# Optimization experiments

Hardware: AMD Instinct MI355X
Metric: run time of the kernel (lower is better)

Reference implementation:

```python
import jax, jax.numpy as jnp
import numpy as np

B, C, N, M_MODES, EMB = 8, 64, 2048, 32, 256
MFREQ = 2 * M_MODES * (2 * M_MODES - 1)  # 4032
SCALE = 1.0 / (C * C)


def setup_inputs() -> dict:
    key = jax.random.key(0)
    ks = jax.random.split(key, 16)
    d = {
        "x": jax.random.normal(ks[0], (B, C, N), jnp.float32),
        "emb": jax.random.normal(ks[1], (B, EMB), jnp.float32),
        "Vf_re": jax.random.normal(ks[2], (MFREQ, N), jnp.float32),
        "Vf_im": jax.random.normal(ks[3], (MFREQ, N), jnp.float32),
        "Vi_re": jax.random.normal(ks[4], (N, MFREQ), jnp.float32),
        "Vi_im": jax.random.normal(ks[5], (N, MFREQ), jnp.float32),
        "w1_re": SCALE * jax.random.uniform(ks[6], (C, C, M_MODES, M_MODES), jnp.float32),
        "w1_im": SCALE * jax.random.uniform(ks[7], (C, C, M_MODES, M_MODES), jnp.float32),
        "w2_re": SCALE * jax.random.uniform(ks[8], (C, C, M_MODES, M_MODES), jnp.float32),
        "w2_im": SCALE * jax.random.uniform(ks[9], (C, C, M_MODES, M_MODES), jnp.float32),
        "m1_re": SCALE * jax.random.uniform(ks[10], (1, M_MODES, M_MODES, EMB), jnp.float32),
        "m1_im": SCALE * jax.random.uniform(ks[11], (1, M_MODES, M_MODES, EMB), jnp.float32),
        "m2_re": SCALE * jax.random.uniform(ks[12], (1, M_MODES, M_MODES, EMB), jnp.float32),
        "m2_im": SCALE * jax.random.uniform(ks[13], (1, M_MODES, M_MODES, EMB), jnp.float32),
    }
    return d


def _spectral_conv(x, emb, Vf, Vi, w1, w2, mod1, mod2):
    m = M_MODES
    # nuft.forward: [B,N,C] complex -> [B,MFREQ,C]
    xc = jnp.transpose(x, (0, 2, 1)).astype(jnp.complex64)
    x_nfft = jnp.einsum('mn,bnc->bmc', Vf, xc)
    # [B,C,2m,2m-1]
    x_ft = jnp.transpose(x_nfft, (0, 2, 1)).reshape(x.shape[0], C, 2 * m, 2 * m - 1)
    embc = emb.astype(jnp.complex64)[:, None, None, :]  # [B,1,1,EMB]
    phi1 = jnp.sum(mod1 * embc, axis=-1)  # [B,m,m]
    phi2 = jnp.sum(mod2 * embc, axis=-1)
    out1 = jnp.einsum('bixy,ioxy->boxy', x_ft[:, :, :m, :m], w1)
    out2 = jnp.einsum('bixy,ioxy->boxy', x_ft[:, :, -m:, :m], w2)
    mod1b = phi1[:, None, :, :] * out1
    mod2b = phi2[:, None, :, :] * out2
    out_ft = jnp.concatenate([mod1b, mod2b], axis=2)  # [B,C,2m,m]
    xf = out_ft.reshape(x.shape[0], C, 2 * m * m)
    # Hermitian-symmetry reconstruction: flip over mode AND channel dims, conj
    xf2 = jnp.conj(jnp.flip(xf[..., 2 * m:], axis=(-2, -1)))
    xf = jnp.concatenate([xf, xf2], axis=-1)  # [B,C,MFREQ]
    xf = jnp.transpose(xf, (0, 2, 1))  # [B,MFREQ,C]
    out = jnp.einsum('nm,bmc->bnc', Vi, xf)  # nuft.inverse -> [B,N,C]
    out = jnp.transpose(out, (0, 2, 1)) / N * 2
    return out.real


def reference(x, emb, Vf_re, Vf_im, Vi_re, Vi_im, w1_re, w1_im, w2_re, w2_im, m1_re, m1_im, m2_re, m2_im):
    Vf = Vf_re + 1j * Vf_im
    Vi = Vi_re + 1j * Vi_im
    w1 = w1_re + 1j * w1_im
    w2 = w2_re + 1j * w2_im
    mod1 = m1_re + 1j * m1_im
    mod2 = m2_re + 1j * m2_im
    return _spectral_conv(x, emb, Vf, Vi, w1, w2, mod1, mod2)
```

## Files before the change

### kernel.cpp

```cpp
#include <hip/hip_runtime.h>

#define BB    8
#define CC    64
#define NN    2048
#define GG    2048
#define MFREQ 4032

typedef __attribute__((ext_vector_type(4))) float f32x4;
typedef __attribute__((ext_vector_type(8))) short bf16x8;

static __device__ __forceinline__ unsigned short f2bf(float f) {
    union { float f; unsigned u; } v; v.f = f;
    unsigned r = v.u + 0x7fff + ((v.u >> 16) & 1);
    return (unsigned short)(r >> 16);
}

static __device__ __forceinline__ bf16x8 as_bf16x8(uint4 u) {
    union { uint4 u; bf16x8 b; } v; v.u = u; return v.b;
}

#define ASYNC_COPY16(gp, lp)                                                        \
    __builtin_amdgcn_global_load_lds(                                               \
        (const __attribute__((address_space(1))) unsigned int*)(gp),                \
        (__attribute__((address_space(3))) unsigned int*)(lp), 16, 0, 0)

__global__ __launch_bounds__(256) void pack_af(const float* __restrict__ vf_re,
                                               const float* __restrict__ vf_im,
                                               unsigned short* __restrict__ af) {
    int idx = blockIdx.x * 256 + threadIdx.x;
    int m = idx >> 9;
    int q = (idx & 511) * 4;
    int g = m & 2047;
    int f = (g >> 5) * 63 + (g & 31);
    const float* src = (m < 2048 ? vf_re : vf_im) + (size_t)f * 2048 + q;
    float4 v = *(const float4*)src;
    ushort4 o; o.x = f2bf(v.x); o.y = f2bf(v.y); o.z = f2bf(v.z); o.w = f2bf(v.w);
    *(ushort4*)(af + (size_t)m * 2048 + q) = o;
}

__global__ __launch_bounds__(256) void pack_xb(const float* __restrict__ x,
                                               unsigned short* __restrict__ xb) {
    int idx = blockIdx.x * 256 + threadIdx.x;
    int q = idx * 4;
    float4 v = *(const float4*)(x + q);
    ushort4 o; o.x = f2bf(v.x); o.y = f2bf(v.y); o.z = f2bf(v.z); o.w = f2bf(v.w);
    *(ushort4*)(xb + q) = o;
}

__global__ __launch_bounds__(256) void pack_mi(const float* __restrict__ vi_re,
                                               const float* __restrict__ vi_im,
                                               unsigned short* __restrict__ mi) {
    int idx = blockIdx.x * 256 + threadIdx.x;
    int n = idx >> 11;
    int q4 = (idx & 2047) * 4;
    int region = q4 >> 11;
    int off = q4 & 2047;
    float4 v;
    if (region == 0) {
        v = *(const float4*)(vi_re + (size_t)n * MFREQ + off);
    } else if (region == 1) {
        float4 t = *(const float4*)(vi_im + (size_t)n * MFREQ + off);
        v.x = -t.x; v.y = -t.y; v.z = -t.z; v.w = -t.w;
    } else {
        if (off < 64) { v.x = v.y = v.z = v.w = 0.0f; }
        else {
            const float* src = (region == 2 ? vi_re : vi_im);
            float4 t = *(const float4*)(src + (size_t)n * MFREQ + (4092 - off));
            v.x = t.w; v.y = t.z; v.z = t.y; v.w = t.x;
        }
    }
    ushort4 o; o.x = f2bf(v.x); o.y = f2bf(v.y); o.z = f2bf(v.z); o.w = f2bf(v.w);
    *(ushort4*)(mi + (size_t)n * 8192 + q4) = o;
}

__global__ __launch_bounds__(256) void pack_wt(const float* __restrict__ w1_re,
                                               const float* __restrict__ w1_im,
                                               const float* __restrict__ w2_re,
                                               const float* __restrict__ w2_im,
                                               unsigned int* __restrict__ wt) {
    __shared__ float sre[64][65];
    __shared__ float sim[64][65];
    int wsel = blockIdx.z;
    const float* wre = wsel ? w2_re : w1_re;
    const float* wim = wsel ? w2_im : w1_im;
    int io0 = blockIdx.y * 64, xy0 = blockIdx.x * 64;
    int t = threadIdx.x;
    int r = t >> 2, cq = (t & 3) * 16;
    for (int j = 0; j < 16; j += 4) {
        float4 a = *(const float4*)(wre + (size_t)(io0 + r) * 1024 + xy0 + cq + j);
        float4 b = *(const float4*)(wim + (size_t)(io0 + r) * 1024 + xy0 + cq + j);
        sre[r][cq + j + 0] = a.x; sre[r][cq + j + 1] = a.y; sre[r][cq + j + 2] = a.z; sre[r][cq + j + 3] = a.w;
        sim[r][cq + j + 0] = b.x; sim[r][cq + j + 1] = b.y; sim[r][cq + j + 2] = b.z; sim[r][cq + j + 3] = b.w;
    }
    __syncthreads();
    int iol = t & 63, gq = t >> 6;
    for (int jj = 0; jj < 16; ++jj) {
        int gl = jj * 4 + gq;
        int g = xy0 + gl + wsel * 1024;
        unsigned int o = (unsigned int)f2bf(sre[iol][gl]) | ((unsigned int)f2bf(sim[iol][gl]) << 16);
        wt[(size_t)g * 4096 + io0 + iol] = o;
    }
}

__global__ __launch_bounds__(256) void phi_k(const float* __restrict__ m1_re,
                                             const float* __restrict__ m1_im,
                                             const float* __restrict__ m2_re,
                                             const float* __restrict__ m2_im,
                                             const float* __restrict__ emb,
                                             float* __restrict__ phi_re,
                                             float* __restrict__ phi_im) {
    int g = blockIdx.x, b = blockIdx.y, e = threadIdx.x;
    int xy = g & 1023;
    const float* mr = (g < 1024 ? m1_re : m2_re) + xy * 256;
    const float* mi = (g < 1024 ? m1_im : m2_im) + xy * 256;
    float em = emb[b * 256 + e];
    float pr = mr[e] * em, pi = mi[e] * em;
    __shared__ float sr[4], si[4];
    for (int s = 32; s > 0; s >>= 1) { pr += __shfl_down(pr, s); pi += __shfl_down(pi, s); }
    int wid = e >> 6;
    if ((e & 63) == 0) { sr[wid] = pr; si[wid] = pi; }
    __syncthreads();
    if (e == 0) {
        phi_re[b * 2048 + g] = sr[0] + sr[1] + sr[2] + sr[3];
        phi_im[b * 2048 + g] = si[0] + si[1] + si[2] + si[3];
    }
}

__global__ __launch_bounds__(256, 2) void gemm_sk(const unsigned short* __restrict__ A,
                                                  const unsigned short* __restrict__ Bm,
                                                  float* __restrict__ P,
                                                  int M, int N, int K, int Kper) {
    __shared__ unsigned short As[128 * 64];
    __shared__ unsigned short Bs[128 * 64];
    int t = threadIdx.x;
    int lane = t & 63, w = t >> 6;
    int m0 = blockIdx.y * 128, n0 = blockIdx.x * 128;
    int z = blockIdx.z;
    int kbase = z * Kper;
    int wm = (w >> 1) * 64, wn = (w & 1) * 64;
    int lr = lane & 15, quad = lane >> 4;
    int rsub = lane >> 3, slot = lane & 7;

    f32x4 acc[4][4] = {};

    for (int kk = kbase; kk < kbase + Kper; kk += 64) {
        __syncthreads();
        #pragma unroll
        for (int l = 0; l < 4; ++l) {
            int r = (w * 4 + l) * 8 + rsub;
            int c = slot ^ (r & 7);
            ASYNC_COPY16(A + (size_t)(m0 + r) * K + kk + c * 8, As + r * 64 + slot * 8);
            ASYNC_COPY16(Bm + (size_t)(n0 + r) * K + kk + c * 8, Bs + r * 64 + slot * 8);
        }
        __syncthreads();
        #pragma unroll
        for (int ks = 0; ks < 2; ++ks) {
            bf16x8 af[4], bfr[4];
            #pragma unroll
            for (int i = 0; i < 4; ++i) {
                int row = wm + i * 16 + lr;
                int q = (ks * 4 + quad) ^ (row & 7);
                af[i] = *(const bf16x8*)(As + row * 64 + q * 8);
                int rowb = wn + i * 16 + lr;
                int qb = (ks * 4 + quad) ^ (rowb & 7);
                bfr[i] = *(const bf16x8*)(Bs + rowb * 64 + qb * 8);
            }
            #pragma unroll
            for (int i = 0; i < 4; ++i)
            #pragma unroll
            for (int j = 0; j < 4; ++j)
                acc[i][j] = __builtin_amdgcn_mfma_f32_16x16x32_bf16(af[i], bfr[j], acc[i][j], 0, 0, 0);
        }
    }
    float* Pz = P + (size_t)z * M * N;
    #pragma unroll
    for (int i = 0; i < 4; ++i)
    #pragma unroll
    for (int j = 0; j < 4; ++j) {
        int rr = m0 + wm + i * 16 + quad * 4;
        int cc = n0 + wn + j * 16 + lr;
        float* cp = Pz + (size_t)rr * N + cc;
        f32x4 v = acc[i][j];
        cp[0]             = v.x;
        cp[(size_t)N]     = v.y;
        cp[2 * (size_t)N] = v.z;
        cp[3 * (size_t)N] = v.w;
    }
}

__global__ __launch_bounds__(256) void reduce_k(const float* __restrict__ P,
                                                float* __restrict__ out,
                                                int S, size_t elems, float alpha) {
    size_t idx = ((size_t)blockIdx.x * 256 + threadIdx.x) * 4;
    float4 s = *(const float4*)(P + idx);
    for (int zz = 1; zz < S; ++zz) {
        float4 v = *(const float4*)(P + (size_t)zz * elems + idx);
        s.x += v.x; s.y += v.y; s.z += v.z; s.w += v.w;
    }
    s.x *= alpha; s.y *= alpha; s.z *= alpha; s.w *= alpha;
    *(float4*)(out + idx) = s;
}

__global__ __launch_bounds__(256) void middle_k(const float* __restrict__ O1,
                                                const unsigned int* __restrict__ wt,
                                                const float* __restrict__ phi_re,
                                                const float* __restrict__ phi_im,
                                                unsigned short* __restrict__ Yt) {
    __shared__ unsigned int wts[4096];
    __shared__ float2 inc[512];
    int g = blockIdx.x, t = threadIdx.x;
    const uint4* wg4 = (const uint4*)(wt + (size_t)g * 4096);
    #pragma unroll
    for (int j = 0; j < 4; ++j) ((uint4*)wts)[t + 256 * j] = wg4[t + 256 * j];
    #pragma unroll
    for (int j = 0; j < 2; ++j) {
        int idx = t + 256 * j;
        float2 a; a.x = O1[(size_t)g * 512 + idx]; a.y = O1[(size_t)(2048 + g) * 512 + idx];
        inc[idx] = a;
    }
    __syncthreads();
    int b = t >> 5, oo = t & 31;
    float ar0 = 0.f, ai0 = 0.f, ar1 = 0.f, ai1 = 0.f;
    #pragma unroll 8
    for (int i = 0; i < 64; ++i) {
        float2 a = inc[b * 64 + i];
        unsigned int u0 = wts[i * 64 + oo];
        unsigned int u1 = wts[i * 64 + oo + 32];
        float w0r = __uint_as_float(u0 << 16);
        float w0i = __uint_as_float(u0 & 0xffff0000u);
        float w1r = __uint_as_float(u1 << 16);
        float w1i = __uint_as_float(u1 & 0xffff0000u);
        ar0 += a.x * w0r - a.y * w0i;  ai0 += a.x * w0i + a.y * w0r;
        ar1 += a.x * w1r - a.y * w1i;  ai1 += a.x * w1i + a.y * w1r;
    }
    float pr = phi_re[b * 2048 + g], pi = phi_im[b * 2048 + g];
    float yr0 = pr * ar0 - pi * ai0, yi0 = pr * ai0 + pi * ar0;
    float yr1 = pr * ar1 - pi * ai1, yi1 = pr * ai1 + pi * ar1;
    {
        size_t r0 = (size_t)(b * 64 + oo) * 8192;
        size_t rf = (size_t)(b * 64 + 63 - oo) * 8192;
        Yt[r0 + g]        = f2bf(yr0);
        Yt[r0 + 2048 + g] = f2bf(yi0);
        Yt[rf + 4096 + g] = f2bf(yr0);
        Yt[rf + 6144 + g] = f2bf(yi0);
    }
    {
        int o = oo + 32;
        size_t r0 = (size_t)(b * 64 + o) * 8192;
        size_t rf = (size_t)(b * 64 + 63 - o) * 8192;
        Yt[r0 + g]        = f2bf(yr1);
        Yt[r0 + 2048 + g] = f2bf(yi1);
        Yt[rf + 4096 + g] = f2bf(yr1);
        Yt[rf + 6144 + g] = f2bf(yi1);
    }
}

extern "C" void kernel_launch(void* const* d_in, const int* in_sizes, int n_in,
                              void* d_out, int out_size, void* d_ws, size_t ws_size,
                              hipStream_t stream) {
    const float* x     = (const float*)d_in[0];
    const float* emb   = (const float*)d_in[1];
    const float* vf_re = (const float*)d_in[2];
    const float* vf_im = (const float*)d_in[3];
    const float* vi_re = (const float*)d_in[4];
    const float* vi_im = (const float*)d_in[5];
    const float* w1_re = (const float*)d_in[6];
    const float* w1_im = (const float*)d_in[7];
    const float* w2_re = (const float*)d_in[8];
    const float* w2_im = (const float*)d_in[9];
    const float* m1_re = (const float*)d_in[10];
    const float* m1_im = (const float*)d_in[11];
    const float* m2_re = (const float*)d_in[12];
    const float* m2_im = (const float*)d_in[13];

    char* ws = (char*)d_ws;
    unsigned short* Af = (unsigned short*)(ws);
    unsigned short* Xb = (unsigned short*)(ws + 16777216);
    unsigned short* Mi = (unsigned short*)(ws + 18874368);
    unsigned int*   Wt = (unsigned int*)(ws + 52428800);
    float*          O1 = (float*)(ws + 85983232);
    float*       PhiRe = (float*)(ws + 94371840);
    float*       PhiIm = (float*)(ws + 94437376);
    unsigned short* Yt = (unsigned short*)(ws + 94502912);
    float*          P  = (float*)(ws + 102891520);
    float* out = (float*)d_out;

    pack_af<<<8192, 256, 0, stream>>>(vf_re, vf_im, Af);
    pack_xb<<<1024, 256, 0, stream>>>(x, Xb);
    pack_mi<<<16384, 256, 0, stream>>>(vi_re, vi_im, Mi);
    pack_wt<<<dim3(16, 64, 2), 256, 0, stream>>>(w1_re, w1_im, w2_re, w2_im, Wt);
    phi_k<<<dim3(2048, 8), 256, 0, stream>>>(m1_re, m1_im, m2_re, m2_im, emb, PhiRe, PhiIm);

    gemm_sk<<<dim3(4, 32, 4), 256, 0, stream>>>(Af, Xb, P, 4096, 512, 2048, 512);
    reduce_k<<<2048, 256, 0, stream>>>(P, O1, 4, (size_t)4096 * 512, 1.0f);

    middle_k<<<2048, 256, 0, stream>>>(O1, Wt, PhiRe, PhiIm, Yt);

    gemm_sk<<<dim3(16, 4, 8), 256, 0, stream>>>(Yt, Mi, P, 512, 2048, 8192, 1024);
    reduce_k<<<1024, 256, 0, stream>>>(P, out, 8, (size_t)512 * 2048, 1.0f / 1024.0f);
}
```

Baseline: 325.7 us.

## Merge pack kernels and batch middle kernel over eight modes with vector stores

```diff
diff --git a/kernel.cpp b/kernel.cpp
--- a/kernel.cpp
+++ b/kernel.cpp
@@ -15,62 +15,59 @@
     return (unsigned short)(r >> 16);
 }
 
-static __device__ __forceinline__ bf16x8 as_bf16x8(uint4 u) {
-    union { uint4 u; bf16x8 b; } v; v.u = u; return v.b;
-}
-
 #define ASYNC_COPY16(gp, lp)                                                        \
     __builtin_amdgcn_global_load_lds(                                               \
         (const __attribute__((address_space(1))) unsigned int*)(gp),                \
         (__attribute__((address_space(3))) unsigned int*)(lp), 16, 0, 0)
 
-__global__ __launch_bounds__(256) void pack_af(const float* __restrict__ vf_re,
-                                               const float* __restrict__ vf_im,
-                                               unsigned short* __restrict__ af) {
-    int idx = blockIdx.x * 256 + threadIdx.x;
-    int m = idx >> 9;
-    int q = (idx & 511) * 4;
-    int g = m & 2047;
-    int f = (g >> 5) * 63 + (g & 31);
-    const float* src = (m < 2048 ? vf_re : vf_im) + (size_t)f * 2048 + q;
-    float4 v = *(const float4*)src;
+__global__ __launch_bounds__(256) void pack_all(const float* __restrict__ vf_re,
+                                                const float* __restrict__ vf_im,
+                                                const float* __restrict__ x,
+                                                const float* __restrict__ vi_re,
+                                                const float* __restrict__ vi_im,
+                                                unsigned short* __restrict__ af,
+                                                unsigned short* __restrict__ xb,
+                                                unsigned short* __restrict__ mi) {
+    int blk = blockIdx.x;
+    float4 v;
+    unsigned short* dst;
+    if (blk < 8192) {
+        int idx = blk * 256 + threadIdx.x;
+        int m = idx >> 9;
+        int q = (idx & 511) * 4;
+        int g = m & 2047;
+        int f = (g >> 5) * 63 + (g & 31);
+        const float* src = (m < 2048 ? vf_re : vf_im) + (size_t)f * 2048 + q;
+        v = *(const float4*)src;
+        dst = af + (size_t)m * 2048 + q;
+    } else if (blk < 9216) {
+        int idx = (blk - 8192) * 256 + threadIdx.x;
+        int q = idx * 4;
+        v = *(const float4*)(x + q);
+        dst = xb + q;
+    } else {
+        int idx = (blk - 9216) * 256 + threadIdx.x;
+        int n = idx >> 11;
+        int q4 = (idx & 2047) * 4;
+        int region = q4 >> 11;
+        int off = q4 & 2047;
+        if (region == 0) {
+            v = *(const float4*)(vi_re + (size_t)n * MFREQ + off);
+        } else if (region == 1) {
+            float4 t = *(const float4*)(vi_im + (size_t)n * MFREQ + off);
+            v.x = -t.x; v.y = -t.y; v.z = -t.z; v.w = -t.w;
+        } else {
+            if (off < 64) { v.x = v.y = v.z = v.w = 0.0f; }
+            else {
+                const float* src = (region == 2 ? vi_re : vi_im);
+                float4 t = *(const float4*)(src + (size_t)n * MFREQ + (4092 - off));
+                v.x = t.w; v.y = t.z; v.z = t.y; v.w = t.x;
+            }
+        }
+        dst = mi + (size_t)n * 8192 + q4;
+    }
     ushort4 o; o.x = f2bf(v.x); o.y = f2bf(v.y); o.z = f2bf(v.z); o.w = f2bf(v.w);
-    *(ushort4*)(af + (size_t)m * 2048 + q) = o;
-}
-
-__global__ __launch_bounds__(256) void pack_xb(const float* __restrict__ x,
-                                               unsigned short* __restrict__ xb) {
-    int idx = blockIdx.x * 256 + threadIdx.x;
-    int q = idx * 4;
-    float4 v = *(const float4*)(x + q);
-    ushort4 o; o.x = f2bf(v.x); o.y = f2bf(v.y); o.z = f2bf(v.z); o.w = f2bf(v.w);
-    *(ushort4*)(xb + q) = o;
-}
-
-__global__ __launch_bounds__(256) void pack_mi(const float* __restrict__ vi_re,
-                                               const float* __restrict__ vi_im,
-                                               unsigned short* __restrict__ mi) {
-    int idx = blockIdx.x * 256 + threadIdx.x;
-    int n = idx >> 11;
-    int q4 = (idx & 2047) * 4;
-    int region = q4 >> 11;
-    int off = q4 & 2047;
-    float4 v;
-    if (region == 0) {
-        v = *(const float4*)(vi_re + (size_t)n * MFREQ + off);
-    } else if (region == 1) {
-        float4 t = *(const float4*)(vi_im + (size_t)n * MFREQ + off);
-        v.x = -t.x; v.y = -t.y; v.z = -t.z; v.w = -t.w;
-    } else {
-        if (off < 64) { v.x = v.y = v.z = v.w = 0.0f; }
-        else {
-            const float* src = (region == 2 ? vi_re : vi_im);
-            float4 t = *(const float4*)(src + (size_t)n * MFREQ + (4092 - off));
-            v.x = t.w; v.y = t.z; v.z = t.y; v.w = t.x;
-        }
-    }
-    ushort4 o; o.x = f2bf(v.x); o.y = f2bf(v.y); o.z = f2bf(v.z); o.w = f2bf(v.w);
-    *(ushort4*)(mi + (size_t)n * 8192 + q4) = o;
+    *(ushort4*)dst = o;
 }
 
 __global__ __launch_bounds__(256) void pack_wt(const float* __restrict__ w1_re,
@@ -206,52 +203,75 @@
                                                 const float* __restrict__ phi_re,
                                                 const float* __restrict__ phi_im,
                                                 unsigned short* __restrict__ Yt) {
-    __shared__ unsigned int wts[4096];
-    __shared__ float2 inc[512];
-    int g = blockIdx.x, t = threadIdx.x;
-    const uint4* wg4 = (const uint4*)(wt + (size_t)g * 4096);
+    __shared__ unsigned int sW[4096];
+    __shared__ float sInc[1024];
+    int t = threadIdx.x;
+    int g0 = blockIdx.x * 8;
+    int b = t >> 5, oo = t & 31;
+
+    unsigned short re0[8], im0[8], re1[8], im1[8];
+
     #pragma unroll
-    for (int j = 0; j < 4; ++j) ((uint4*)wts)[t + 256 * j] = wg4[t + 256 * j];
-    #pragma unroll
-    for (int j = 0; j < 2; ++j) {
-        int idx = t + 256 * j;
-        float2 a; a.x = O1[(size_t)g * 512 + idx]; a.y = O1[(size_t)(2048 + g) * 512 + idx];
-        inc[idx] = a;
-    }
-    __syncthreads();
-    int b = t >> 5, oo = t & 31;
-    float ar0 = 0.f, ai0 = 0.f, ar1 = 0.f, ai1 = 0.f;
-    #pragma unroll 8
-    for (int i = 0; i < 64; ++i) {
-        float2 a = inc[b * 64 + i];
-        unsigned int u0 = wts[i * 64 + oo];
-        unsigned int u1 = wts[i * 64 + oo + 32];
-        float w0r = __uint_as_float(u0 << 16);
-        float w0i = __uint_as_float(u0 & 0xffff0000u);
-        float w1r = __uint_as_float(u1 << 16);
-        float w1i = __uint_as_float(u1 & 0xffff0000u);
-        ar0 += a.x * w0r - a.y * w0i;  ai0 += a.x * w0i + a.y * w0r;
-        ar1 += a.x * w1r - a.y * w1i;  ai1 += a.x * w1i + a.y * w1r;
-    }
-    float pr = phi_re[b * 2048 + g], pi = phi_im[b * 2048 + g];
-    float yr0 = pr * ar0 - pi * ai0, yi0 = pr * ai0 + pi * ar0;
-    float yr1 = pr * ar1 - pi * ai1, yi1 = pr * ai1 + pi * ar1;
+    for (int gt = 0; gt < 8; ++gt) {
+        int g = g0 + gt;
+        __syncthreads();
+        #pragma unroll
+        for (int j = 0; j < 4; ++j)
+            ASYNC_COPY16(wt + (size_t)g * 4096 + (j * 256 + t) * 4, sW + (j * 256 + t) * 4);
+        {
+            const float* src = (t < 128) ? (O1 + (size_t)g * 512 + t * 4)
+                                         : (O1 + (size_t)(2048 + g) * 512 + (t - 128) * 4);
+            ASYNC_COPY16(src, sInc + t * 4);
+        }
+        __syncthreads();
+
+        float ar0 = 0.f, ai0 = 0.f, ar1 = 0.f, ai1 = 0.f;
+        #pragma unroll 8
+        for (int i = 0; i < 64; ++i) {
+            float ax = sInc[b * 64 + i];
+            float ay = sInc[512 + b * 64 + i];
+            unsigned int u0 = sW[i * 64 + oo];
+            unsigned int u1 = sW[i * 64 + oo + 32];
+            float w0r = __uint_as_float(u0 << 16);
+            float w0i = __uint_as_float(u0 & 0xffff0000u);
+            float w1r = __uint_as_float(u1 << 16);
+            float w1i = __uint_as_float(u1 & 0xffff0000u);
+            ar0 += ax * w0r - ay * w0i;  ai0 += ax * w0i + ay * w0r;
+            ar1 += ax * w1r - ay * w1i;  ai1 += ax * w1i + ay * w1r;
+        }
+        float pr = phi_re[b * 2048 + g], pi = phi_im[b * 2048 + g];
+        re0[gt] = f2bf(pr * ar0 - pi * ai0);
+        im0[gt] = f2bf(pr * ai0 + pi * ar0);
+        re1[gt] = f2bf(pr * ar1 - pi * ai1);
+        im1[gt] = f2bf(pr * ai1 + pi * ar1);
+    }
+
+    uint4 vre0, vim0, vre1, vim1;
+    vre0.x = re0[0] | (re0[1] << 16); vre0.y = re0[2] | (re0[3] << 16);
+    vre0.z = re0[4] | (re0[5] << 16); vre0.w = re0[6] | (re0[7] << 16);
+    vim0.x = im0[0] | (im0[1] << 16); vim0.y = im0[2] | (im0[3] << 16);
+    vim0.z = im0[4] | (im0[5] << 16); vim0.w = im0[6] | (im0[7] << 16);
+    vre1.x = re1[0] | (re1[1] << 16); vre1.y = re1[2] | (re1[3] << 16);
+    vre1.z = re1[4] | (re1[5] << 16); vre1.w = re1[6] | (re1[7] << 16);
+    vim1.x = im1[0] | (im1[1] << 16); vim1.y = im1[2] | (im1[3] << 16);
+    vim1.z = im1[4] | (im1[5] << 16); vim1.w = im1[6] | (im1[7] << 16);
+
     {
         size_t r0 = (size_t)(b * 64 + oo) * 8192;
         size_t rf = (size_t)(b * 64 + 63 - oo) * 8192;
-        Yt[r0 + g]        = f2bf(yr0);
-        Yt[r0 + 2048 + g] = f2bf(yi0);
-        Yt[rf + 4096 + g] = f2bf(yr0);
-        Yt[rf + 6144 + g] = f2bf(yi0);
+        *(uint4*)(Yt + r0 + g0)        = vre0;
+        *(uint4*)(Yt + r0 + 2048 + g0) = vim0;
+        *(uint4*)(Yt + rf + 4096 + g0) = vre0;
+        *(uint4*)(Yt + rf + 6144 + g0) = vim0;
     }
     {
         int o = oo + 32;
         size_t r0 = (size_t)(b * 64 + o) * 8192;
         size_t rf = (size_t)(b * 64 + 63 - o) * 8192;
-        Yt[r0 + g]        = f2bf(yr1);
-        Yt[r0 + 2048 + g] = f2bf(yi1);
-        Yt[rf + 4096 + g] = f2bf(yr1);
-        Yt[rf + 6144 + g] = f2bf(yi1);
+        *(uint4*)(Yt + r0 + g0)        = vre1;
+        *(uint4*)(Yt + r0 + 2048 + g0) = vim1;
+        *(uint4*)(Yt + rf + 4096 + g0) = vre1;
+        *(uint4*)(Yt + rf + 6144 + g0) = vim1;
     }
 }
 
@@ -285,16 +305,14 @@
     float*          P  = (float*)(ws + 102891520);
     float* out = (float*)d_out;
 
-    pack_af<<<8192, 256, 0, stream>>>(vf_re, vf_im, Af);
-    pack_xb<<<1024, 256, 0, stream>>>(x, Xb);
-    pack_mi<<<16384, 256, 0, stream>>>(vi_re, vi_im, Mi);
+    pack_all<<<25600, 256, 0, stream>>>(vf_re, vf_im, x, vi_re, vi_im, Af, Xb, Mi);
     pack_wt<<<dim3(16, 64, 2), 256, 0, stream>>>(w1_re, w1_im, w2_re, w2_im, Wt);
     phi_k<<<dim3(2048, 8), 256, 0, stream>>>(m1_re, m1_im, m2_re, m2_im, emb, PhiRe, PhiIm);
 
     gemm_sk<<<dim3(4, 32, 4), 256, 0, stream>>>(Af, Xb, P, 4096, 512, 2048, 512);
     reduce_k<<<2048, 256, 0, stream>>>(P, O1, 4, (size_t)4096 * 512, 1.0f);
 
-    middle_k<<<2048, 256, 0, stream>>>(O1, Wt, PhiRe, PhiIm, Yt);
+    middle_k<<<256, 256, 0, stream>>>(O1, Wt, PhiRe, PhiIm, Yt);
 
     gemm_sk<<<dim3(16, 4, 8), 256, 0, stream>>>(Yt, Mi, P, 512, 2048, 8192, 1024);
     reduce_k<<<1024, 256, 0, stream>>>(P, out, 8, (size_t)512 * 2048, 1.0f / 1024.0f);
```

New measurement: 331.9 us. No clear change (+1.9%).
